# Kernel optimization log

Measured on AMD Instinct MI355X. Metric: run time of the kernel, lower is better.

The kernel has to match this reference:

```python
import jax, jax.numpy as jnp
import numpy as np

N = 100000        # nodes
E = 1600000       # edges
D_IN = 128
D_H = 128
D_OUT = 47        # classes
BN_EPS = 1e-5


def _gcn_norm(edge_index):
    # PyG GCNConv default: add self-loops, symmetric deg^{-1/2} normalization.
    src = jnp.concatenate([edge_index[0], jnp.arange(N, dtype=edge_index.dtype)])
    dst = jnp.concatenate([edge_index[1], jnp.arange(N, dtype=edge_index.dtype)])
    deg = jax.ops.segment_sum(jnp.ones_like(dst, dtype=jnp.float32), dst, num_segments=N)
    dinv = jnp.where(deg > 0, jax.lax.rsqrt(deg), 0.0)
    norm = dinv[src] * dinv[dst]  # [E+N]
    return src, dst, norm


def _gcn_conv(x, W, b, src, dst, norm):
    h = x @ W                                    # [N, out]
    msg = h[src] * norm[:, None]                 # gather + scale  [E+N, out]
    out = jax.ops.segment_sum(msg, dst, num_segments=N)  # scatter-add
    return out + b


def _batchnorm(h, gamma, beta):
    # BatchNorm1d training-mode math over the node dimension (deterministic).
    mean = jnp.mean(h, axis=0)
    var = jnp.mean(jnp.square(h - mean), axis=0)
    return (h - mean) * jax.lax.rsqrt(var + BN_EPS) * gamma + beta


def setup_inputs() -> dict:
    key = jax.random.key(0)
    ks = jax.random.split(key, 10)
    x = jax.random.normal(ks[0], (N, D_IN), jnp.float32)
    edge_index = jax.random.randint(ks[1], (2, E), 0, N, dtype=jnp.int32)
    s = 1.0 / np.sqrt(D_H)
    W0 = jax.random.uniform(ks[2], (D_IN, D_H), jnp.float32, -s, s)
    b0 = jnp.zeros((D_H,), jnp.float32)
    Wm = jax.random.uniform(ks[3], (D_H, D_H), jnp.float32, -s, s)
    bm = jnp.zeros((D_H,), jnp.float32)
    Wl = jax.random.uniform(ks[4], (D_H, D_OUT), jnp.float32, -s, s)
    bl = jnp.zeros((D_OUT,), jnp.float32)
    g0 = jnp.ones((D_H,), jnp.float32); be0 = jnp.zeros((D_H,), jnp.float32)
    g1 = jnp.ones((D_H,), jnp.float32); be1 = jnp.zeros((D_H,), jnp.float32)
    return {"x": x, "edge_index": edge_index, "W0": W0, "b0": b0,
            "Wm": Wm, "bm": bm, "Wl": Wl, "bl": bl,
            "g0": g0, "be0": be0, "g1": g1, "be1": be1}


def reference(x, edge_index, W0, b0, Wm, bm, Wl, bl, g0, be0, g1, be1):
    src, dst, norm = _gcn_norm(edge_index)
    # layer 0: conv -> BN -> ReLU (dropout = identity in eval)
    h = _gcn_conv(x, W0, b0, src, dst, norm)
    h = jax.nn.relu(_batchnorm(h, g0, be0))
    # mid layer
    h = _gcn_conv(h, Wm, bm, src, dst, norm)
    h = jax.nn.relu(_batchnorm(h, g1, be1))
    # last conv + log_softmax over classes
    h = _gcn_conv(h, Wl, bl, src, dst, norm)
    return jax.nn.log_softmax(h, axis=1)
```

## Files before the change

### kernel.cpp

```cpp
#include <hip/hip_runtime.h>
#include <hip/hip_bf16.h>

#define NN 100000
#define NE 1600000
#define NBKT 196
#define CAP 10240

typedef __hip_bfloat16 bf16;
typedef __attribute__((ext_vector_type(8))) __bf16 bf16x8;
typedef __attribute__((ext_vector_type(4))) float f32x4;

__device__ __forceinline__ float ldf(const void* p, long i, int isbf) {
  if (isbf) return __bfloat162float(((const bf16*)p)[i]);
  return ((const float*)p)[i];
}
__device__ __forceinline__ float bflo(unsigned u) { return __uint_as_float(u << 16); }
__device__ __forceinline__ float bfhi(unsigned u) { return __uint_as_float(u & 0xffff0000u); }
__device__ __forceinline__ unsigned short f2b(float v) {
  bf16 h = __float2bfloat16(v);
  return __builtin_bit_cast(unsigned short, h);
}
__device__ __forceinline__ unsigned pack2(float lo, float hi) {
  return (unsigned)f2b(lo) | ((unsigned)f2b(hi) << 16);
}
__device__ __forceinline__ void acc8(float* s, uint4 a) {
  s[0] += bflo(a.x); s[1] += bfhi(a.x);
  s[2] += bflo(a.y); s[3] += bfhi(a.y);
  s[4] += bflo(a.z); s[5] += bfhi(a.z);
  s[6] += bflo(a.w); s[7] += bfhi(a.w);
}

__global__ void k_init(const void* __restrict__ g0, int* __restrict__ flag,
                       int* __restrict__ gcur) {
  int t = threadIdx.x;
  if (t == 0) {
    unsigned u = *(const unsigned*)g0;
    flag[0] = (u == 0x3F800000u) ? 0 : 1;
  }
  if (t < NBKT) gcur[t] = t * CAP;
}

__global__ void k_wprep(const void* __restrict__ W0, const void* __restrict__ Wm,
                        const void* __restrict__ Wl, unsigned short* __restrict__ WT0,
                        unsigned short* __restrict__ WTm, unsigned short* __restrict__ WTl,
                        const int* __restrict__ flag) {
  const int isbf = flag[0];
  for (int idx = blockIdx.x * 256 + threadIdx.x; idx < 16384 * 2 + 48 * 128;
       idx += gridDim.x * 256) {
    if (idx < 16384) {
      int c = idx >> 7, k = idx & 127;
      WT0[idx] = f2b(ldf(W0, (long)k * 128 + c, isbf));
    } else if (idx < 32768) {
      int j = idx - 16384;
      int c = j >> 7, k = j & 127;
      WTm[j] = f2b(ldf(Wm, (long)k * 128 + c, isbf));
    } else {
      int j = idx - 32768;
      int c = j >> 7, k = j & 127;
      WTl[j] = (c < 47) ? f2b(ldf(Wl, (long)k * 47 + c, isbf)) : 0;
    }
  }
}

__global__ void k_bucketA(const int* __restrict__ ei, int* __restrict__ gcur,
                          unsigned* __restrict__ ebuf) {
  __shared__ int lcnt[NBKT], lbase[NBKT];
  for (int j = threadIdx.x; j < NBKT; j += 256) lcnt[j] = 0;
  __syncthreads();
  int t = blockIdx.x * 256 + threadIdx.x;
  long base = (long)t * 8;
  int s[8], d[8], n = 0;
  if (base + 7 < NE) {
    int4 s0 = ((const int4*)ei)[2 * t];
    int4 s1 = ((const int4*)ei)[2 * t + 1];
    int4 d0 = ((const int4*)(ei + NE))[2 * t];
    int4 d1 = ((const int4*)(ei + NE))[2 * t + 1];
    s[0] = s0.x; s[1] = s0.y; s[2] = s0.z; s[3] = s0.w;
    s[4] = s1.x; s[5] = s1.y; s[6] = s1.z; s[7] = s1.w;
    d[0] = d0.x; d[1] = d0.y; d[2] = d0.z; d[3] = d0.w;
    d[4] = d1.x; d[5] = d1.y; d[6] = d1.z; d[7] = d1.w;
    n = 8;
  } else {
    for (long e = base; e < NE; ++e) {
      s[n] = ei[e];
      d[n] = ei[NE + e];
      n++;
    }
  }
  for (int j = 0; j < n; ++j) atomicAdd(&lcnt[d[j] >> 9], 1);
  __syncthreads();
  for (int j = threadIdx.x; j < NBKT; j += 256) {
    int c = lcnt[j];
    lbase[j] = (c > 0) ? atomicAdd(&gcur[j], c) : 0;
    lcnt[j] = 0;
  }
  __syncthreads();
  for (int j = 0; j < n; ++j) {
    int b = d[j] >> 9;
    int off = atomicAdd(&lcnt[b], 1);
    int pos = lbase[b] + off;
    if (pos < (b + 1) * CAP)
      ebuf[pos] = ((unsigned)s[j] << 9) | (unsigned)(d[j] & 511);
  }
}

__global__ void k_bktscan(const int* __restrict__ gcur, int* __restrict__ bbase) {
  __shared__ int sm[256];
  int t = threadIdx.x;
  int c = (t < NBKT) ? min(gcur[t] - t * CAP, CAP) : 0;
  sm[t] = c;
  __syncthreads();
  for (int off = 1; off < 256; off <<= 1) {
    int v = (t >= off) ? sm[t - off] : 0;
    __syncthreads();
    sm[t] += v;
    __syncthreads();
  }
  if (t < NBKT) bbase[t] = sm[t] - c;
}

__global__ __launch_bounds__(256) void k_sortB(
    const unsigned* __restrict__ ebuf, const int* __restrict__ gcur,
    const int* __restrict__ bbase, int* __restrict__ rowptr,
    float* __restrict__ dinv, int* __restrict__ srcs) {
  __shared__ int hist[512];
  __shared__ int tmp[256];
  __shared__ int stage[CAP];
  int b = blockIdx.x, t = threadIdx.x;
  int n0 = b << 9;
  int cnt = min(gcur[b] - b * CAP, CAP);
  int base = bbase[b];
  const unsigned* E = ebuf + (long)b * CAP;
  hist[t] = 0;
  hist[t + 256] = 0;
  __syncthreads();
  for (int idx = t; idx < cnt; idx += 256) atomicAdd(&hist[E[idx] & 511], 1);
  __syncthreads();
  int a0 = hist[2 * t], a1 = hist[2 * t + 1];
  tmp[t] = a0 + a1;
  __syncthreads();
  for (int off = 1; off < 256; off <<= 1) {
    int v = (t >= off) ? tmp[t - off] : 0;
    __syncthreads();
    tmp[t] += v;
    __syncthreads();
  }
  int pb = tmp[t] - (a0 + a1);
  int i0 = n0 + 2 * t, i1 = i0 + 1;
  if (i0 < NN) {
    rowptr[i0] = base + pb;
    dinv[i0] = rsqrtf((float)(a0 + 1));
  }
  if (i1 < NN) {
    rowptr[i1] = base + pb + a0;
    dinv[i1] = rsqrtf((float)(a1 + 1));
  }
  if (b == NBKT - 1 && t == 0) rowptr[NN] = base + cnt;
  hist[2 * t] = pb;
  hist[2 * t + 1] = pb + a0;
  __syncthreads();
  for (int idx = t; idx < cnt; idx += 256) {
    unsigned u = E[idx];
    int p = atomicAdd(&hist[u & 511], 1);
    stage[p] = (int)(u >> 9);
  }
  __syncthreads();
  for (int idx = t; idx < cnt; idx += 256) srcs[base + idx] = stage[idx];
}


template <int NT, int MODE, int OST>
__global__ __launch_bounds__(256) void k_gemm_reg(
    const void* __restrict__ Aptr, const unsigned short* __restrict__ WT,
    const float* __restrict__ stats, const void* __restrict__ g,
    const void* __restrict__ be, const float* __restrict__ dinv,
    unsigned* __restrict__ Cp, const int* __restrict__ flag) {
  __shared__ float sss[256];
  const int isbf = flag[0];
  if (MODE == 1) {
    int t = threadIdx.x;
    if (t < 128) {
      float mean = stats[t] * (1.0f / NN);
      float var = stats[128 + t] * (1.0f / NN) - mean * mean;
      float sc = ldf(g, t, isbf) * rsqrtf(var + 1e-5f);
      sss[t] = sc;
      sss[128 + t] = ldf(be, t, isbf) - mean * sc;
    }
    __syncthreads();
  }
  const int lane = threadIdx.x & 63, w = threadIdx.x >> 6;
  const int m = lane & 15, q = lane >> 4;
  const int rbase = blockIdx.x * 64 + w * 16;
  const int row = min(rbase + m, NN - 1);

  f32x4 acc[NT];
#pragma unroll
  for (int t = 0; t < NT; t++) acc[t] = (f32x4){0.f, 0.f, 0.f, 0.f};

#pragma unroll
  for (int kc = 0; kc < 128; kc += 32) {
    bf16x8 av;
    if (MODE == 0) {
      if (isbf) {
        uint4 u = ((const uint4*)Aptr)[(long)row * 16 + kc / 8 + q];
        av = __builtin_bit_cast(bf16x8, u);
      } else {
        float4 f0 = ((const float4*)Aptr)[(long)row * 32 + kc / 4 + q * 2];
        float4 f1 = ((const float4*)Aptr)[(long)row * 32 + kc / 4 + q * 2 + 1];
        uint4 u;
        u.x = pack2(f0.x, f0.y); u.y = pack2(f0.z, f0.w);
        u.z = pack2(f1.x, f1.y); u.w = pack2(f1.z, f1.w);
        av = __builtin_bit_cast(bf16x8, u);
      }
    } else {
      uint4 u = ((const uint4*)Aptr)[(long)row * 16 + kc / 8 + q];
      int k0 = kc + q * 8;
      float f0 = fmaxf(bflo(u.x) * sss[k0 + 0] + sss[128 + k0 + 0], 0.f);
      float f1 = fmaxf(bfhi(u.x) * sss[k0 + 1] + sss[128 + k0 + 1], 0.f);
      float f2 = fmaxf(bflo(u.y) * sss[k0 + 2] + sss[128 + k0 + 2], 0.f);
      float f3 = fmaxf(bfhi(u.y) * sss[k0 + 3] + sss[128 + k0 + 3], 0.f);
      float f4 = fmaxf(bflo(u.z) * sss[k0 + 4] + sss[128 + k0 + 4], 0.f);
      float f5 = fmaxf(bfhi(u.z) * sss[k0 + 5] + sss[128 + k0 + 5], 0.f);
      float f6 = fmaxf(bflo(u.w) * sss[k0 + 6] + sss[128 + k0 + 6], 0.f);
      float f7 = fmaxf(bfhi(u.w) * sss[k0 + 7] + sss[128 + k0 + 7], 0.f);
      uint4 p;
      p.x = pack2(f0, f1); p.y = pack2(f2, f3);
      p.z = pack2(f4, f5); p.w = pack2(f6, f7);
      av = __builtin_bit_cast(bf16x8, p);
    }
#pragma unroll
    for (int t = 0; t < NT; t++) {
      bf16x8 bv = *(const bf16x8*)&WT[(t * 16 + m) * 128 + kc + q * 8];
      acc[t] = __builtin_amdgcn_mfma_f32_16x16x32_bf16(av, bv, acc[t], 0, 0, 0);
    }
  }

  float dv[4];
  int gr[4];
#pragma unroll
  for (int reg = 0; reg < 4; reg++) {
    gr[reg] = rbase + q * 4 + reg;
    dv[reg] = dinv[min(gr[reg], NN - 1)];
  }
#pragma unroll
  for (int t = 0; t < NT; t++) {
#pragma unroll
    for (int reg = 0; reg < 4; reg++) {
      float v = acc[t][reg] * dv[reg];
      float p = __shfl_xor(v, 1);
      if (!(m & 1) && gr[reg] < NN) {
        Cp[(long)gr[reg] * OST + t * 8 + (m >> 1)] = pack2(v, p);
      }
    }
  }
  if (OST > NT * 8) {
    constexpr int PAD = OST - NT * 8;
    for (int z = lane; z < 16 * PAD; z += 64) {
      int rr = z / PAD, u = NT * 8 + z % PAD;
      int grow = rbase + rr;
      if (grow < NN) Cp[(long)grow * OST + u] = 0;
    }
  }
}


__global__ void k_gather128(const uint4* __restrict__ hp4, const int* __restrict__ rowptr,
                            const int* __restrict__ srcs, const float* __restrict__ dinv,
                            const void* __restrict__ bias, uint4* __restrict__ convp4,
                            const int* __restrict__ flag) {
  int lane = threadIdx.x & 63;
  int i = blockIdx.x * 4 + (threadIdx.x >> 6);
  if (i >= NN) return;
  int eg = lane >> 4, g = lane & 15;
  float s[8] = {0.f, 0.f, 0.f, 0.f, 0.f, 0.f, 0.f, 0.f};
  if (eg == 0) acc8(s, hp4[(long)i * 16 + g]);
  int e0 = rowptr[i], e1 = rowptr[i + 1];
  int e = e0;
  for (; e + 8 <= e1; e += 8) {
    int i0 = srcs[e + eg], i1 = srcs[e + 4 + eg];
    uint4 a0 = hp4[(long)i0 * 16 + g];
    uint4 a1 = hp4[(long)i1 * 16 + g];
    acc8(s, a0);
    acc8(s, a1);
  }
  for (; e < e1; e += 4) {
    int idx = e + eg;
    if (idx < e1) acc8(s, hp4[(long)srcs[idx] * 16 + g]);
  }
#pragma unroll
  for (int j = 0; j < 8; j++) {
    s[j] += __shfl_xor(s[j], 32);
    s[j] += __shfl_xor(s[j], 16);
  }
  if (eg == 0) {
    float dv = dinv[i];
    int isbf = flag[0];
    uint4 o;
    o.x = pack2(s[0] * dv + ldf(bias, 8 * g + 0, isbf), s[1] * dv + ldf(bias, 8 * g + 1, isbf));
    o.y = pack2(s[2] * dv + ldf(bias, 8 * g + 2, isbf), s[3] * dv + ldf(bias, 8 * g + 3, isbf));
    o.z = pack2(s[4] * dv + ldf(bias, 8 * g + 4, isbf), s[5] * dv + ldf(bias, 8 * g + 5, isbf));
    o.w = pack2(s[6] * dv + ldf(bias, 8 * g + 6, isbf), s[7] * dv + ldf(bias, 8 * g + 7, isbf));
    convp4[(long)i * 16 + g] = o;
  }
}


__global__ void k_bnstats(const uint2* __restrict__ conv2, float* __restrict__ stats) {
  __shared__ float4 sS[256], sQ[256];
  int t = threadIdx.x;
  int c4 = t & 31, rg = t >> 5;
  float4 s = {0.f, 0.f, 0.f, 0.f}, q = {0.f, 0.f, 0.f, 0.f};
  for (int r = blockIdx.x * 8 + rg; r < NN; r += 256 * 8) {
    uint2 u = conv2[(long)r * 32 + c4];
    float v0 = bflo(u.x), v1 = bfhi(u.x), v2 = bflo(u.y), v3 = bfhi(u.y);
    s.x += v0; s.y += v1; s.z += v2; s.w += v3;
    q.x += v0 * v0; q.y += v1 * v1; q.z += v2 * v2; q.w += v3 * v3;
  }
  sS[t] = s; sQ[t] = q;
  __syncthreads();
  for (int off = 128; off >= 32; off >>= 1) {
    if (t < off) {
      float4 a = sS[t + off], b = sQ[t + off];
      sS[t].x += a.x; sS[t].y += a.y; sS[t].z += a.z; sS[t].w += a.w;
      sQ[t].x += b.x; sQ[t].y += b.y; sQ[t].z += b.z; sQ[t].w += b.w;
    }
    __syncthreads();
  }
  if (t < 32) {
    float4 a = sS[t], b = sQ[t];
    atomicAdd(&stats[t * 4 + 0], a.x);
    atomicAdd(&stats[t * 4 + 1], a.y);
    atomicAdd(&stats[t * 4 + 2], a.z);
    atomicAdd(&stats[t * 4 + 3], a.w);
    atomicAdd(&stats[128 + t * 4 + 0], b.x);
    atomicAdd(&stats[128 + t * 4 + 1], b.y);
    atomicAdd(&stats[128 + t * 4 + 2], b.z);
    atomicAdd(&stats[128 + t * 4 + 3], b.w);
  }
}


__global__ void k_gather_out(const uint4* __restrict__ h2p4,
                             const int* __restrict__ rowptr,
                             const int* __restrict__ srcs, const float* __restrict__ dinv,
                             const void* __restrict__ bl, float* __restrict__ out,
                             const int* __restrict__ flag) {
  int lane = threadIdx.x & 63;
  int i = blockIdx.x * 4 + (threadIdx.x >> 6);
  if (i >= NN) return;
  int eg = lane >> 3, g = lane & 7;
  float s[8] = {0.f, 0.f, 0.f, 0.f, 0.f, 0.f, 0.f, 0.f};
  if (eg == 0) acc8(s, h2p4[(long)i * 8 + g]);
  int e0 = rowptr[i], e1 = rowptr[i + 1];
  int e = e0;
  for (; e + 16 <= e1; e += 16) {
    int i0 = srcs[e + eg], i1 = srcs[e + 8 + eg];
    uint4 a0 = h2p4[(long)i0 * 8 + g];
    uint4 a1 = h2p4[(long)i1 * 8 + g];
    acc8(s, a0);
    acc8(s, a1);
  }
  for (; e < e1; e += 8) {
    int idx = e + eg;
    if (idx < e1) acc8(s, h2p4[(long)srcs[idx] * 8 + g]);
  }
#pragma unroll
  for (int j = 0; j < 8; j++) {
    s[j] += __shfl_xor(s[j], 32);
    s[j] += __shfl_xor(s[j], 16);
    s[j] += __shfl_xor(s[j], 8);
  }
  float dv = dinv[i];
  int isbf = flag[0];
  float v[8];
  float mloc = -1e30f;
#pragma unroll
  for (int j = 0; j < 8; j++) {
    int c = 8 * g + j;
    v[j] = (c < 47) ? s[j] * dv + ldf(bl, c, isbf) : -1e30f;
    mloc = fmaxf(mloc, v[j]);
  }
  mloc = fmaxf(mloc, __shfl_xor(mloc, 1));
  mloc = fmaxf(mloc, __shfl_xor(mloc, 2));
  mloc = fmaxf(mloc, __shfl_xor(mloc, 4));
  float ex = 0.f;
#pragma unroll
  for (int j = 0; j < 8; j++) {
    int c = 8 * g + j;
    if (c < 47) ex += expf(v[j] - mloc);
  }
  ex += __shfl_xor(ex, 1);
  ex += __shfl_xor(ex, 2);
  ex += __shfl_xor(ex, 4);
  float ls = logf(ex);
  if (eg == 0) {
#pragma unroll
    for (int j = 0; j < 8; j++) {
      int c = 8 * g + j;
      if (c < 47) out[(long)i * 47 + c] = v[j] - mloc - ls;
    }
  }
}


extern "C" void kernel_launch(void* const* d_in, const int* in_sizes, int n_in,
                              void* d_out, int out_size, void* d_ws, size_t ws_size,
                              hipStream_t stream) {
  const void* x = d_in[0];
  const int* ei = (const int*)d_in[1];
  const void* W0 = d_in[2];
  const void* b0 = d_in[3];
  const void* Wm = d_in[4];
  const void* bm = d_in[5];
  const void* Wl = d_in[6];
  const void* bl = d_in[7];
  const void* g0 = d_in[8];
  const void* be0 = d_in[9];
  const void* g1 = d_in[10];
  const void* be1 = d_in[11];
  float* out = (float*)d_out;

  char* ws = (char*)d_ws;
  size_t off = 0;
  auto alloc = [&](size_t b) {
    void* p = ws + off;
    off += (b + 255) & ~(size_t)255;
    return p;
  };
  int* flag = (int*)alloc(256);
  int* gcur = (int*)alloc(256 * 4);
  int* bbase = (int*)alloc(256 * 4);
  int* rowptr = (int*)alloc((NN + 1) * 4);
  float* dinv = (float*)alloc(NN * 4);
  int* srcs = (int*)alloc((size_t)NE * 4);
  unsigned* ebuf = (unsigned*)alloc((size_t)NBKT * CAP * 4);
  unsigned short* WT0 = (unsigned short*)alloc(16384 * 2);
  unsigned short* WTm = (unsigned short*)alloc(16384 * 2);
  unsigned short* WTl = (unsigned short*)alloc(48 * 128 * 2);
  unsigned* hp = (unsigned*)alloc((size_t)NN * 64 * 4);
  unsigned* convp = (unsigned*)alloc((size_t)NN * 64 * 4);
  float* stats = (float*)alloc(512 * 4);
  unsigned* h2p = hp;

  hipMemsetAsync(stats, 0, 512 * 4, stream);

  k_init<<<1, 256, 0, stream>>>(g0, flag, gcur);
  k_wprep<<<64, 256, 0, stream>>>(W0, Wm, Wl, WT0, WTm, WTl, flag);
  int nge8 = (NE / 8 + 255) / 256;
  k_bucketA<<<nge8, 256, 0, stream>>>(ei, gcur, ebuf);
  k_bktscan<<<1, 256, 0, stream>>>(gcur, bbase);
  k_sortB<<<NBKT, 256, 0, stream>>>(ebuf, gcur, bbase, rowptr, dinv, srcs);

  int ngemm = (NN + 63) / 64;
  int ngath = (NN + 3) / 4;
  k_gemm_reg<8, 0, 64><<<ngemm, 256, 0, stream>>>(x, WT0, nullptr, nullptr, nullptr,
                                                  dinv, hp, flag);
  k_gather128<<<ngath, 256, 0, stream>>>((const uint4*)hp, rowptr, srcs, dinv, b0,
                                         (uint4*)convp, flag);
  k_bnstats<<<256, 256, 0, stream>>>((const uint2*)convp, stats);

  k_gemm_reg<8, 1, 64><<<ngemm, 256, 0, stream>>>(convp, WTm, stats, g0, be0,
                                                  dinv, hp, flag);
  k_gather128<<<ngath, 256, 0, stream>>>((const uint4*)hp, rowptr, srcs, dinv, bm,
                                         (uint4*)convp, flag);
  k_bnstats<<<256, 256, 0, stream>>>((const uint2*)convp, stats + 256);

  k_gemm_reg<3, 1, 32><<<ngemm, 256, 0, stream>>>(convp, WTl, stats + 256, g1, be1,
                                                  dinv, h2p, flag);
  k_gather_out<<<ngath, 256, 0, stream>>>((const uint4*)h2p, rowptr, srcs, dinv, bl,
                                          out, flag);
}
```

Measured before the change: 551.6 us.

## Split gather by feature halves, preload edge indices via shuffles, shrink output row stride

The 128-wide gather now runs twice as many blocks, each handling one half of the feature columns, so 8 edges are processed per wave step with 8 lanes per half-row. Each wave loads up to 64 source indices at once and broadcasts them with shuffles instead of re-reading the index array per edge. The final layer stores rows with a stride of 24 words (48 bf16) instead of 32, which cuts gather traffic, and the explicit padding write is removed. The risk is that the edge-index and rowptr loads are repeated per half, and the 12-byte unaligned loads in the output gather may vectorise poorly.

```diff
diff --git a/kernel.cpp b/kernel.cpp
--- a/kernel.cpp
+++ b/kernel.cpp
@@ -253,54 +253,64 @@
       }
     }
   }
-  if (OST > NT * 8) {
-    constexpr int PAD = OST - NT * 8;
-    for (int z = lane; z < 16 * PAD; z += 64) {
-      int rr = z / PAD, u = NT * 8 + z % PAD;
-      int grow = rbase + rr;
-      if (grow < NN) Cp[(long)grow * OST + u] = 0;
-    }
-  }
 }
 
 
 __global__ void k_gather128(const uint4* __restrict__ hp4, const int* __restrict__ rowptr,
                             const int* __restrict__ srcs, const float* __restrict__ dinv,
                             const void* __restrict__ bias, uint4* __restrict__ convp4,
-                            const int* __restrict__ flag) {
+                            const int* __restrict__ flag, int nblk) {
+  int u = blockIdx.x;
+  int half = (u >= nblk) ? 1 : 0;
+  int nb = u - half * nblk;
   int lane = threadIdx.x & 63;
-  int i = blockIdx.x * 4 + (threadIdx.x >> 6);
+  int i = nb * 4 + (threadIdx.x >> 6);
   if (i >= NN) return;
-  int eg = lane >> 4, g = lane & 15;
+  int e0 = rowptr[i], e1 = rowptr[i + 1];
+  int deg = e1 - e0;
+  int sidx = (lane < deg) ? srcs[e0 + lane] : 0;
+  int eg = lane >> 3, g = lane & 7;
+  int go = half * 8 + g;
   float s[8] = {0.f, 0.f, 0.f, 0.f, 0.f, 0.f, 0.f, 0.f};
-  if (eg == 0) acc8(s, hp4[(long)i * 16 + g]);
-  int e0 = rowptr[i], e1 = rowptr[i + 1];
-  int e = e0;
-  for (; e + 8 <= e1; e += 8) {
-    int i0 = srcs[e + eg], i1 = srcs[e + 4 + eg];
-    uint4 a0 = hp4[(long)i0 * 16 + g];
-    uint4 a1 = hp4[(long)i1 * 16 + g];
+  if (eg == 0) acc8(s, hp4[(long)i * 16 + go]);
+  int dcap = min(deg, 64);
+  int e = 0;
+  for (; e + 16 <= dcap; e += 16) {
+    int i0 = __shfl(sidx, e + eg);
+    int i1 = __shfl(sidx, e + 8 + eg);
+    uint4 a0 = hp4[(long)i0 * 16 + go];
+    uint4 a1 = hp4[(long)i1 * 16 + go];
     acc8(s, a0);
     acc8(s, a1);
   }
-  for (; e < e1; e += 4) {
+  for (; e + 8 <= dcap; e += 8) {
+    int i0 = __shfl(sidx, e + eg);
+    acc8(s, hp4[(long)i0 * 16 + go]);
+  }
+  if (e < dcap) {
     int idx = e + eg;
-    if (idx < e1) acc8(s, hp4[(long)srcs[idx] * 16 + g]);
+    int i0 = __shfl(sidx, min(idx, dcap - 1));
+    if (idx < dcap) acc8(s, hp4[(long)i0 * 16 + go]);
+  }
+  for (int ee = 64 + eg; ee < deg; ee += 8) {
+    acc8(s, hp4[(long)srcs[e0 + ee] * 16 + go]);
   }
 #pragma unroll
   for (int j = 0; j < 8; j++) {
     s[j] += __shfl_xor(s[j], 32);
     s[j] += __shfl_xor(s[j], 16);
+    s[j] += __shfl_xor(s[j], 8);
   }
   if (eg == 0) {
     float dv = dinv[i];
     int isbf = flag[0];
+    int cb = go * 8;
     uint4 o;
-    o.x = pack2(s[0] * dv + ldf(bias, 8 * g + 0, isbf), s[1] * dv + ldf(bias, 8 * g + 1, isbf));
-    o.y = pack2(s[2] * dv + ldf(bias, 8 * g + 2, isbf), s[3] * dv + ldf(bias, 8 * g + 3, isbf));
-    o.z = pack2(s[4] * dv + ldf(bias, 8 * g + 4, isbf), s[5] * dv + ldf(bias, 8 * g + 5, isbf));
-    o.w = pack2(s[6] * dv + ldf(bias, 8 * g + 6, isbf), s[7] * dv + ldf(bias, 8 * g + 7, isbf));
-    convp4[(long)i * 16 + g] = o;
+    o.x = pack2(s[0] * dv + ldf(bias, cb + 0, isbf), s[1] * dv + ldf(bias, cb + 1, isbf));
+    o.y = pack2(s[2] * dv + ldf(bias, cb + 2, isbf), s[3] * dv + ldf(bias, cb + 3, isbf));
+    o.z = pack2(s[4] * dv + ldf(bias, cb + 4, isbf), s[5] * dv + ldf(bias, cb + 5, isbf));
+    o.w = pack2(s[6] * dv + ldf(bias, cb + 6, isbf), s[7] * dv + ldf(bias, cb + 7, isbf));
+    convp4[(long)i * 16 + go] = o;
   }
 }
 
@@ -340,7 +350,7 @@
 }
 
 
-__global__ void k_gather_out(const uint4* __restrict__ h2p4,
+__global__ void k_gather_out(const unsigned* __restrict__ h2p,
                              const int* __restrict__ rowptr,
                              const int* __restrict__ srcs, const float* __restrict__ dinv,
                              const void* __restrict__ bl, float* __restrict__ out,
@@ -348,35 +358,70 @@
   int lane = threadIdx.x & 63;
   int i = blockIdx.x * 4 + (threadIdx.x >> 6);
   if (i >= NN) return;
+  int e0 = rowptr[i], e1 = rowptr[i + 1];
+  int deg = e1 - e0;
+  int sidx = (lane < deg) ? srcs[e0 + lane] : 0;
   int eg = lane >> 3, g = lane & 7;
-  float s[8] = {0.f, 0.f, 0.f, 0.f, 0.f, 0.f, 0.f, 0.f};
-  if (eg == 0) acc8(s, h2p4[(long)i * 8 + g]);
-  int e0 = rowptr[i], e1 = rowptr[i + 1];
-  int e = e0;
-  for (; e + 16 <= e1; e += 16) {
-    int i0 = srcs[e + eg], i1 = srcs[e + 8 + eg];
-    uint4 a0 = h2p4[(long)i0 * 8 + g];
-    uint4 a1 = h2p4[(long)i1 * 8 + g];
-    acc8(s, a0);
-    acc8(s, a1);
-  }
-  for (; e < e1; e += 8) {
+  float s[6] = {0.f, 0.f, 0.f, 0.f, 0.f, 0.f};
+  if (eg == 0) {
+    const unsigned* p = h2p + (long)i * 24 + 3 * g;
+    unsigned x = p[0], y = p[1], z = p[2];
+    s[0] += bflo(x); s[1] += bfhi(x);
+    s[2] += bflo(y); s[3] += bfhi(y);
+    s[4] += bflo(z); s[5] += bfhi(z);
+  }
+  int dcap = min(deg, 64);
+  int e = 0;
+  for (; e + 16 <= dcap; e += 16) {
+    int i0 = __shfl(sidx, e + eg);
+    int i1 = __shfl(sidx, e + 8 + eg);
+    const unsigned* p0 = h2p + (long)i0 * 24 + 3 * g;
+    const unsigned* p1 = h2p + (long)i1 * 24 + 3 * g;
+    unsigned x0 = p0[0], y0 = p0[1], z0 = p0[2];
+    unsigned x1 = p1[0], y1 = p1[1], z1 = p1[2];
+    s[0] += bflo(x0) + bflo(x1); s[1] += bfhi(x0) + bfhi(x1);
+    s[2] += bflo(y0) + bflo(y1); s[3] += bfhi(y0) + bfhi(y1);
+    s[4] += bflo(z0) + bflo(z1); s[5] += bfhi(z0) + bfhi(z1);
+  }
+  for (; e + 8 <= dcap; e += 8) {
+    int i0 = __shfl(sidx, e + eg);
+    const unsigned* p0 = h2p + (long)i0 * 24 + 3 * g;
+    unsigned x = p0[0], y = p0[1], z = p0[2];
+    s[0] += bflo(x); s[1] += bfhi(x);
+    s[2] += bflo(y); s[3] += bfhi(y);
+    s[4] += bflo(z); s[5] += bfhi(z);
+  }
+  if (e < dcap) {
     int idx = e + eg;
-    if (idx < e1) acc8(s, h2p4[(long)srcs[idx] * 8 + g]);
-  }
-#pragma unroll
-  for (int j = 0; j < 8; j++) {
+    int i0 = __shfl(sidx, min(idx, dcap - 1));
+    if (idx < dcap) {
+      const unsigned* p0 = h2p + (long)i0 * 24 + 3 * g;
+      unsigned x = p0[0], y = p0[1], z = p0[2];
+      s[0] += bflo(x); s[1] += bfhi(x);
+      s[2] += bflo(y); s[3] += bfhi(y);
+      s[4] += bflo(z); s[5] += bfhi(z);
+    }
+  }
+  for (int ee = 64 + eg; ee < deg; ee += 8) {
+    const unsigned* p0 = h2p + (long)srcs[e0 + ee] * 24 + 3 * g;
+    unsigned x = p0[0], y = p0[1], z = p0[2];
+    s[0] += bflo(x); s[1] += bfhi(x);
+    s[2] += bflo(y); s[3] += bfhi(y);
+    s[4] += bflo(z); s[5] += bfhi(z);
+  }
+#pragma unroll
+  for (int j = 0; j < 6; j++) {
     s[j] += __shfl_xor(s[j], 32);
     s[j] += __shfl_xor(s[j], 16);
     s[j] += __shfl_xor(s[j], 8);
   }
   float dv = dinv[i];
   int isbf = flag[0];
-  float v[8];
+  float v[6];
   float mloc = -1e30f;
 #pragma unroll
-  for (int j = 0; j < 8; j++) {
-    int c = 8 * g + j;
+  for (int j = 0; j < 6; j++) {
+    int c = 6 * g + j;
     v[j] = (c < 47) ? s[j] * dv + ldf(bl, c, isbf) : -1e30f;
     mloc = fmaxf(mloc, v[j]);
   }
@@ -385,8 +430,8 @@
   mloc = fmaxf(mloc, __shfl_xor(mloc, 4));
   float ex = 0.f;
 #pragma unroll
-  for (int j = 0; j < 8; j++) {
-    int c = 8 * g + j;
+  for (int j = 0; j < 6; j++) {
+    int c = 6 * g + j;
     if (c < 47) ex += expf(v[j] - mloc);
   }
   ex += __shfl_xor(ex, 1);
@@ -395,8 +440,8 @@
   float ls = logf(ex);
   if (eg == 0) {
 #pragma unroll
-    for (int j = 0; j < 8; j++) {
-      int c = 8 * g + j;
+    for (int j = 0; j < 6; j++) {
+      int c = 6 * g + j;
       if (c < 47) out[(long)i * 47 + c] = v[j] - mloc - ls;
     }
   }
@@ -455,18 +500,17 @@
   int ngath = (NN + 3) / 4;
   k_gemm_reg<8, 0, 64><<<ngemm, 256, 0, stream>>>(x, WT0, nullptr, nullptr, nullptr,
                                                   dinv, hp, flag);
-  k_gather128<<<ngath, 256, 0, stream>>>((const uint4*)hp, rowptr, srcs, dinv, b0,
-                                         (uint4*)convp, flag);
+  k_gather128<<<2 * ngath, 256, 0, stream>>>((const uint4*)hp, rowptr, srcs, dinv, b0,
+                                             (uint4*)convp, flag, ngath);
   k_bnstats<<<256, 256, 0, stream>>>((const uint2*)convp, stats);
 
   k_gemm_reg<8, 1, 64><<<ngemm, 256, 0, stream>>>(convp, WTm, stats, g0, be0,
                                                   dinv, hp, flag);
-  k_gather128<<<ngath, 256, 0, stream>>>((const uint4*)hp, rowptr, srcs, dinv, bm,
-                                         (uint4*)convp, flag);
+  k_gather128<<<2 * ngath, 256, 0, stream>>>((const uint4*)hp, rowptr, srcs, dinv, bm,
+                                             (uint4*)convp, flag, ngath);
   k_bnstats<<<256, 256, 0, stream>>>((const uint2*)convp, stats + 256);
 
-  k_gemm_reg<3, 1, 32><<<ngemm, 256, 0, stream>>>(convp, WTl, stats + 256, g1, be1,
+  k_gemm_reg<3, 1, 24><<<ngemm, 256, 0, stream>>>(convp, WTl, stats + 256, g1, be1,
                                                   dinv, h2p, flag);
-  k_gather_out<<<ngath, 256, 0, stream>>>((const uint4*)h2p, rowptr, srcs, dinv, bl,
-                                          out, flag);
-}
+  k_gather_out<<<ngath, 256, 0, stream>>>(h2p, rowptr, srcs, dinv, bl, out, flag);
+}
```

Measured after the change: 550.2 us. About the same (-0.3%).
